# Kernel tuning notes

Measured on AMD Instinct MI355X. Metric: run time of the kernel, lower is better.

## Reference

```python
import jax, jax.numpy as jnp
import numpy as np

N_TREE = 200
DEPTH = 3
N_LEAF = 2 ** (DEPTH + 1) - 1      # 15 internal decision nodes
N_LEAVES = N_LEAF + 1              # 16 leaves
N_NODE = 64
BATCH = 2048
D_FEAT = 512
LR = 0.01


def _leaf_paths(depth):
    """For each of the 2^(depth+1) leaves, the internal-node index and the
    left/right bit at every level (matches the tf.gather index construction:
    bit==0 -> take p, bit==1 -> take 1-p; children of node n are 2n+1, 2n+2)."""
    L = 2 ** (depth + 1)
    nodes = np.zeros((L, depth + 1), np.int32)
    bits = np.zeros((L, depth + 1), np.int32)
    for l in range(L):
        node = 0
        for d in range(depth + 1):
            bit = (l >> (depth - d)) & 1
            nodes[l, d] = node
            bits[l, d] = bit
            node = 2 * node + 1 + bit
    return nodes, bits

_NODES, _BITS = _leaf_paths(DEPTH)


def setup_inputs() -> dict:
    key = jax.random.key(0)
    ks = jax.random.split(key, 9)
    u = lambda k, s: jax.random.uniform(k, s, jnp.float32, -0.05, 0.05)  # keras 'uniform' init
    return {
        "x": jax.random.normal(ks[0], (BATCH, D_FEAT), jnp.float32),
        "y_true": jax.random.normal(ks[1], (BATCH, 1), jnp.float32),
        "w_t": u(ks[2], (N_TREE, D_FEAT, N_NODE)),
        "b_t": u(ks[3], (N_TREE, N_NODE)),
        "w_d": u(ks[4], (N_TREE, N_NODE, N_LEAF)),
        "b_d": u(ks[5], (N_TREE, N_LEAF)),
        "w_l": u(ks[6], (N_TREE, N_LEAVES)),
        "b_l": u(ks[7], (N_TREE,)),
        "f_0": jnp.full((1,), 0.5, jnp.float32),
    }


def reference(x, y_true, w_t, b_t, w_d, b_d, w_l, b_l, f_0):
    B = x.shape[0]
    # Batched per-tree small MLP (the 200-iteration Python loop in the original).
    # Dropout is identity at inference.
    h = jax.nn.relu(jnp.einsum('bd,tdn->tbn', x, w_t) + b_t[:, None, :])        # [T,B,N_NODE]
    p = jax.nn.sigmoid(jnp.einsum('tbn,tnl->tbl', h, w_d) + b_d[:, None, :])    # [T,B,15]
    # Soft binary-tree routing: mu[t,b,leaf] = prod over path of p or (1-p).
    # This reproduces the tiled-index tf.gather construction exactly.
    pn = p[..., _NODES]                                                         # [T,B,16,DEPTH+1]
    q = jnp.where(_BITS == 1, 1.0 - pn, pn)
    mu = jnp.prod(q, axis=-1)                                                   # [T,B,16]
    # Per-tree leaf score with tanh.
    f = jnp.tanh(jnp.einsum('tbl,tl->tb', mu, w_l) + b_l[:, None])              # [T,B]
    # Sequential boosting accumulation: predict_k = f_0 + lr * sum_{i<k} f_i.
    cum = f_0 + LR * jnp.cumsum(f.T, axis=1)                                    # [B,T]
    py_x = jnp.concatenate([jnp.broadcast_to(f_0[None, :], (B, 1)), cum], axis=1)  # [B,T+1]
    return py_x
```

## Files before the change

kernel.cpp:

```cpp
#include <hip/hip_runtime.h>

#define T_TREES 200
#define BATCH   2048
#define D_FEAT  512
#define N_NODE  64
#define LR      0.01f

typedef __attribute__((__ext_vector_type__(8)))  __bf16 bf16x8;
typedef __attribute__((__ext_vector_type__(16))) float  f32x16;

__device__ __forceinline__ unsigned short f32_to_bf16(float f) {
    unsigned u = __float_as_uint(f);
    u += 0x7FFFu + ((u >> 16) & 1u);
    return (unsigned short)(u >> 16);
}

__device__ __forceinline__ void gload_lds16(const void* g, void* l) {
    __builtin_amdgcn_global_load_lds(
        (__attribute__((address_space(1))) void*)(void*)g,
        (__attribute__((address_space(3))) void*)l,
        16, 0, 0);
}

__global__ __launch_bounds__(256) void prep_all(
    const float* __restrict__ x, const float* __restrict__ w_t,
    const float* __restrict__ w_d,
    unsigned short* __restrict__ x_p, unsigned short* __restrict__ w_p,
    unsigned short* __restrict__ w_dt) {
    __shared__ float tile[64 * 65];
    int b = blockIdx.x;
    if (b < 256) {
        int mb = b >> 3, slab = b & 7;
        const float* src = x + (mb * 64) * D_FEAT + slab * 64;
        #pragma unroll
        for (int p = 0; p < 16; ++p) {
            int idx = p * 256 + threadIdx.x;
            int r = idx >> 6, c = idx & 63;
            tile[r * 65 + c] = src[r * D_FEAT + c];
        }
        __syncthreads();
        int mt = mb >> 1, mq = mb & 1;
        unsigned short* dst = x_p + mt * 65536 + slab * 8192 + mq * 512;
        #pragma unroll
        for (int p = 0; p < 2; ++p) {
            int sid = p * 256 + threadIdx.x;
            int kgl = sid >> 6;
            int r   = sid & 63;
            const float* sr = &tile[r * 65 + kgl * 8];
            bf16x8 o;
            #pragma unroll
            for (int j = 0; j < 8; ++j) o[j] = (__bf16)sr[j];
            *(bf16x8*)(dst + kgl * 1024 + r * 8) = o;
        }
    } else if (b < 1856) {
        int bb = b - 256;
        int t = bb >> 3, slab = bb & 7;
        const float* src = w_t + t * (D_FEAT * N_NODE) + slab * 64 * N_NODE;
        #pragma unroll
        for (int p = 0; p < 16; ++p) {
            int idx = p * 256 + threadIdx.x;
            int d = idx >> 6, n = idx & 63;
            tile[d * 65 + n] = src[d * N_NODE + n];
        }
        __syncthreads();
        unsigned short* dst = w_p + (t >> 1) * 65536 + slab * 8192 + (t & 1) * 512;
        #pragma unroll
        for (int p = 0; p < 2; ++p) {
            int sid = p * 256 + threadIdx.x;
            int kgl = sid >> 6;
            int n   = sid & 63;
            bf16x8 o;
            #pragma unroll
            for (int j = 0; j < 8; ++j) o[j] = (__bf16)tile[(kgl * 8 + j) * 65 + n];
            *(bf16x8*)(dst + kgl * 1024 + n * 8) = o;
        }
    } else {
        int i = (b - 1856) * 256 + threadIdx.x;
        int n = i & 63;
        int l = (i >> 6) & 31;
        int t = i >> 11;
        float v = (l < 15) ? w_d[(t * 64 + n) * 15 + l] : 0.f;
        w_dt[i] = f32_to_bf16(v);
    }
}

__global__ __launch_bounds__(256, 4) void gbdt_main(
    const unsigned short* __restrict__ x_p,
    const unsigned short* __restrict__ w_p,
    const unsigned short* __restrict__ w_dt,
    const float* __restrict__ b_t,
    const float* __restrict__ b_d,
    const float* __restrict__ w_l,
    const float* __restrict__ b_l,
    float* __restrict__ f_ws)
{
    __shared__ alignas(16) char smem[34816];
    unsigned short* Hs = (unsigned short*)smem;
    __bf16*         Hb = (__bf16*)smem;
    float*          Pf = (float*)smem;

    const int tid    = threadIdx.x;
    const int lane   = tid & 63;
    const int w      = tid >> 6;
    const int lane31 = lane & 31;
    const int kh     = lane >> 5;
    const int wm     = w >> 1;
    const int wn     = w & 1;

    const int xcd  = blockIdx.x & 7;
    const int slot = blockIdx.x >> 3;
    const int mt   = slot & 15;
    const int pj   = slot >> 4;
    const int pair = xcd * 13 + pj;
    if (pair >= 100) return;
    const int t0 = pair * 2;
    const int m0 = mt * 128;

    const char* ga = (const char*)(x_p + mt * 65536) + tid * 16;
    const char* gb = (const char*)(w_p + pair * 65536) + tid * 16;

    const int aoff = kh * 2048 + (wm * 64 + lane31) * 16;
    const int boff = 8192 + kh * 2048 + (wn * 64 + lane31) * 16;

    f32x16 acc[2][2];
    #pragma unroll
    for (int mb = 0; mb < 2; ++mb)
        #pragma unroll
        for (int nb = 0; nb < 2; ++nb)
            acc[mb][nb] = (f32x16)(0.f);

#define STAGE(cn, base) do {                                              \
        gload_lds16(ga + (cn) * 8192,        (base) + tid * 16);          \
        gload_lds16(ga + (cn) * 8192 + 4096, (base) + tid * 16 + 4096);   \
        gload_lds16(gb + (cn) * 8192,        (base) + 8192 + tid * 16);   \
        gload_lds16(gb + (cn) * 8192 + 4096, (base) + 8192 + tid * 16 + 4096); \
    } while (0)

    STAGE(0, smem);

    for (int c = 0; c < 16; ++c) {
        __syncthreads();
        if (c < 15) STAGE(c + 1, smem + ((c + 1) & 1) * 16384);
        const char* base = smem + (c & 1) * 16384;
        __builtin_amdgcn_s_setprio(1);
        #pragma unroll
        for (int s2 = 0; s2 < 2; ++s2) {
            bf16x8 av0 = *(const bf16x8*)(base + aoff + s2 * 4096);
            bf16x8 av1 = *(const bf16x8*)(base + aoff + s2 * 4096 + 512);
            bf16x8 bv0 = *(const bf16x8*)(base + boff + s2 * 4096);
            bf16x8 bv1 = *(const bf16x8*)(base + boff + s2 * 4096 + 512);
            acc[0][0] = __builtin_amdgcn_mfma_f32_32x32x16_bf16(av0, bv0, acc[0][0], 0, 0, 0);
            acc[0][1] = __builtin_amdgcn_mfma_f32_32x32x16_bf16(av0, bv1, acc[0][1], 0, 0, 0);
            acc[1][0] = __builtin_amdgcn_mfma_f32_32x32x16_bf16(av1, bv0, acc[1][0], 0, 0, 0);
            acc[1][1] = __builtin_amdgcn_mfma_f32_32x32x16_bf16(av1, bv1, acc[1][1], 0, 0, 0);
        }
        __builtin_amdgcn_s_setprio(0);
    }

    __syncthreads();

    #pragma unroll
    for (int nb = 0; nb < 2; ++nb) {
        float btv = b_t[(t0 + wn) * 64 + nb * 32 + lane31];
        #pragma unroll
        for (int mb = 0; mb < 2; ++mb)
            #pragma unroll
            for (int r = 0; r < 16; ++r) {
                int m = wm * 64 + mb * 32 + (r & 3) + 8 * (r >> 2) + 4 * kh;
                float h = fmaxf(acc[mb][nb][r] + btv, 0.f);
                Hb[wn * 8704 + m * 68 + nb * 32 + lane31] = (__bf16)h;
            }
    }
    __syncthreads();

    f32x16 acc2[2] = { (f32x16)(0.f), (f32x16)(0.f) };
    const unsigned short* pW = w_dt + (t0 + wn) * 2048 + lane31 * 64 + kh * 8;
    __builtin_amdgcn_s_setprio(1);
    #pragma unroll
    for (int s = 0; s < 4; ++s) {
        bf16x8 bv = *(const bf16x8*)(pW + s * 16);
        #pragma unroll
        for (int i = 0; i < 2; ++i) {
            const unsigned short* pH =
                Hs + wn * 8704 + (wm * 64 + i * 32 + lane31) * 68 + s * 16 + kh * 8;
            bf16x8 av = *(const bf16x8*)pH;
            acc2[i] = __builtin_amdgcn_mfma_f32_32x32x16_bf16(av, bv, acc2[i], 0, 0, 0);
        }
    }
    __builtin_amdgcn_s_setprio(0);
    __syncthreads();

    if (lane31 < 15) {
        float bdv = b_d[(t0 + wn) * 15 + lane31];
        #pragma unroll
        for (int i = 0; i < 2; ++i)
            #pragma unroll
            for (int r = 0; r < 16; ++r) {
                int m = wm * 64 + i * 32 + (r & 3) + 8 * (r >> 2) + 4 * kh;
                float lg = acc2[i][r] + bdv;
                Pf[(wn * 128 + m) * 17 + lane31] = 1.f / (1.f + __expf(-lg));
            }
    }
    __syncthreads();

    {
        int m = tid & 127;
        int j = tid >> 7;
        int t = t0 + j;
        float pv[15];
        #pragma unroll
        for (int i = 0; i < 15; ++i) pv[i] = Pf[(j * 128 + m) * 17 + i];
        float facc = 0.f;
        #pragma unroll
        for (int leaf = 0; leaf < 16; ++leaf) {
            float mu = 1.f;
            int node = 0;
            #pragma unroll
            for (int d = 0; d < 4; ++d) {
                int bit = (leaf >> (3 - d)) & 1;
                float p = pv[node];
                mu *= bit ? (1.f - p) : p;
                node = 2 * node + 1 + bit;
            }
            facc += mu * w_l[t * 16 + leaf];
        }
        f_ws[(m0 + m) * T_TREES + t] = tanhf(facc + b_l[t]);
    }
#undef STAGE
}

__global__ __launch_bounds__(256) void scan_k(const float* __restrict__ f_ws,
                                              const float* __restrict__ f0p,
                                              float* __restrict__ out) {
    int lane = threadIdx.x & 63, wid = threadIdx.x >> 6;
    int b = blockIdx.x * 4 + wid;
    float f0 = f0p[0];
    float4 v;
    if (lane < 50) v = *(const float4*)(f_ws + b * T_TREES + lane * 4);
    else           v = make_float4(0.f, 0.f, 0.f, 0.f);
    float p0 = v.x;
    float p1 = p0 + v.y;
    float p2 = p1 + v.z;
    float p3 = p2 + v.w;
    float s = p3;
    #pragma unroll
    for (int off = 1; off < 64; off <<= 1) {
        float y = __shfl_up(s, off, 64);
        if (lane >= off) s += y;
    }
    float excl = s - p3;
    if (lane < 50) {
        float* o = out + b * (T_TREES + 1) + 1 + lane * 4;
        o[0] = f0 + LR * (excl + p0);
        o[1] = f0 + LR * (excl + p1);
        o[2] = f0 + LR * (excl + p2);
        o[3] = f0 + LR * (excl + p3);
    }
    if (lane == 0) out[b * (T_TREES + 1)] = f0;
}

extern "C" void kernel_launch(void* const* d_in, const int* in_sizes, int n_in,
                              void* d_out, int out_size, void* d_ws, size_t ws_size,
                              hipStream_t stream) {
    const float* x   = (const float*)d_in[0];
    const float* w_t = (const float*)d_in[2];
    const float* b_t = (const float*)d_in[3];
    const float* w_d = (const float*)d_in[4];
    const float* b_d = (const float*)d_in[5];
    const float* w_l = (const float*)d_in[6];
    const float* b_l = (const float*)d_in[7];
    const float* f_0 = (const float*)d_in[8];
    float* out = (float*)d_out;

    char* ws = (char*)d_ws;
    unsigned short* x_p  = (unsigned short*)(ws);
    unsigned short* w_p  = (unsigned short*)(ws + 2097152);
    unsigned short* w_dt = (unsigned short*)(ws + 15204352);
    float*          f_ws = (float*)(ws + 16023552);

    prep_all<<<3456, 256, 0, stream>>>(x, w_t, w_d, x_p, w_p, w_dt);
    gbdt_main<<<1664, 256, 0, stream>>>(x_p, w_p, w_dt, b_t, b_d, w_l, b_l, f_ws);
    scan_k<<<512, 256, 0, stream>>>(f_ws, f_0, out);
}
```

Measured before the change: 133.0 us.

## Double block M-tile to 256 rows and add triple-buffered K pipeline

Each block now has 512 threads and covers 256 batch rows per tree pair instead of 128. Each tree's weight tile is therefore staged once for twice as many rows, halving weight traffic per output. The K loop switches from a double buffer with __syncthreads to a three-stage LDS ring of 64-wide K chunks. It uses explicit vmcnt waits and a single barrier, keeping two chunks in flight. The cost is 144 KB of LDS per block, which allows only one block per CU, and half as many blocks in the grid, so there is less latency hiding from concurrent blocks.

```diff
diff --git a/kernel.cpp b/kernel.cpp
--- a/kernel.cpp
+++ b/kernel.cpp
@@ -84,7 +84,7 @@
     }
 }
 
-__global__ __launch_bounds__(256, 4) void gbdt_main(
+__global__ __launch_bounds__(512, 2) void gbdt_main(
     const unsigned short* __restrict__ x_p,
     const unsigned short* __restrict__ w_p,
     const unsigned short* __restrict__ w_dt,
@@ -94,7 +94,7 @@
     const float* __restrict__ b_l,
     float* __restrict__ f_ws)
 {
-    __shared__ alignas(16) char smem[34816];
+    __shared__ alignas(16) char smem[147456];
     unsigned short* Hs = (unsigned short*)smem;
     __bf16*         Hb = (__bf16*)smem;
     float*          Pf = (float*)smem;
@@ -109,18 +109,19 @@
 
     const int xcd  = blockIdx.x & 7;
     const int slot = blockIdx.x >> 3;
-    const int mt   = slot & 15;
-    const int pj   = slot >> 4;
+    const int mt8  = slot & 7;
+    const int pj   = slot >> 3;
     const int pair = xcd * 13 + pj;
     if (pair >= 100) return;
     const int t0 = pair * 2;
-    const int m0 = mt * 128;
-
-    const char* ga = (const char*)(x_p + mt * 65536) + tid * 16;
-    const char* gb = (const char*)(w_p + pair * 65536) + tid * 16;
-
-    const int aoff = kh * 2048 + (wm * 64 + lane31) * 16;
-    const int boff = 8192 + kh * 2048 + (wn * 64 + lane31) * 16;
+    const int m0 = mt8 * 256;
+
+    const char* ga0 = (const char*)(x_p + (2 * mt8 + 0) * 65536) + tid * 16;
+    const char* ga1 = (const char*)(x_p + (2 * mt8 + 1) * 65536) + tid * 16;
+    const char* gb  = (const char*)(w_p + pair * 65536) + tid * 16;
+
+    const int aoff = (wm >> 1) * 16384 + kh * 2048 + ((wm & 1) * 64 + lane31) * 16;
+    const int boff = 32768 + kh * 2048 + (wn * 64 + lane31) * 16;
 
     f32x16 acc[2][2];
     #pragma unroll
@@ -129,32 +130,42 @@
         for (int nb = 0; nb < 2; ++nb)
             acc[mb][nb] = (f32x16)(0.f);
 
-#define STAGE(cn, base) do {                                              \
-        gload_lds16(ga + (cn) * 8192,        (base) + tid * 16);          \
-        gload_lds16(ga + (cn) * 8192 + 4096, (base) + tid * 16 + 4096);   \
-        gload_lds16(gb + (cn) * 8192,        (base) + 8192 + tid * 16);   \
-        gload_lds16(gb + (cn) * 8192 + 4096, (base) + 8192 + tid * 16 + 4096); \
+#define STAGE(kt, base) do {                                               \
+        gload_lds16(ga0 + (kt) * 16384,        (base) + tid * 16);         \
+        gload_lds16(ga0 + (kt) * 16384 + 8192, (base) + 8192  + tid * 16); \
+        gload_lds16(ga1 + (kt) * 16384,        (base) + 16384 + tid * 16); \
+        gload_lds16(ga1 + (kt) * 16384 + 8192, (base) + 24576 + tid * 16); \
+        gload_lds16(gb  + (kt) * 16384,        (base) + 32768 + tid * 16); \
+        gload_lds16(gb  + (kt) * 16384 + 8192, (base) + 40960 + tid * 16); \
     } while (0)
 
-    STAGE(0, smem);
-
-    for (int c = 0; c < 16; ++c) {
-        __syncthreads();
-        if (c < 15) STAGE(c + 1, smem + ((c + 1) & 1) * 16384);
-        const char* base = smem + (c & 1) * 16384;
+    char* b0 = smem;
+    char* b1 = smem + 49152;
+    char* b2 = smem + 98304;
+
+    STAGE(0, b0);
+    STAGE(1, b1);
+
+    #pragma unroll
+    for (int kt = 0; kt < 8; ++kt) {
+        if (kt < 7) asm volatile("s_waitcnt vmcnt(6)" ::: "memory");
+        else        asm volatile("s_waitcnt vmcnt(0)" ::: "memory");
+        __builtin_amdgcn_s_barrier();
+        if (kt < 6) STAGE(kt + 2, b2);
         __builtin_amdgcn_s_setprio(1);
         #pragma unroll
-        for (int s2 = 0; s2 < 2; ++s2) {
-            bf16x8 av0 = *(const bf16x8*)(base + aoff + s2 * 4096);
-            bf16x8 av1 = *(const bf16x8*)(base + aoff + s2 * 4096 + 512);
-            bf16x8 bv0 = *(const bf16x8*)(base + boff + s2 * 4096);
-            bf16x8 bv1 = *(const bf16x8*)(base + boff + s2 * 4096 + 512);
+        for (int ks = 0; ks < 4; ++ks) {
+            bf16x8 av0 = *(const bf16x8*)(b0 + aoff + ks * 4096);
+            bf16x8 av1 = *(const bf16x8*)(b0 + aoff + ks * 4096 + 512);
+            bf16x8 bv0 = *(const bf16x8*)(b0 + boff + ks * 4096);
+            bf16x8 bv1 = *(const bf16x8*)(b0 + boff + ks * 4096 + 512);
             acc[0][0] = __builtin_amdgcn_mfma_f32_32x32x16_bf16(av0, bv0, acc[0][0], 0, 0, 0);
             acc[0][1] = __builtin_amdgcn_mfma_f32_32x32x16_bf16(av0, bv1, acc[0][1], 0, 0, 0);
             acc[1][0] = __builtin_amdgcn_mfma_f32_32x32x16_bf16(av1, bv0, acc[1][0], 0, 0, 0);
             acc[1][1] = __builtin_amdgcn_mfma_f32_32x32x16_bf16(av1, bv1, acc[1][1], 0, 0, 0);
         }
         __builtin_amdgcn_s_setprio(0);
+        char* t = b0; b0 = b1; b1 = b2; b2 = t;
     }
 
     __syncthreads();
@@ -167,8 +178,8 @@
             #pragma unroll
             for (int r = 0; r < 16; ++r) {
                 int m = wm * 64 + mb * 32 + (r & 3) + 8 * (r >> 2) + 4 * kh;
-                float h = fmaxf(acc[mb][nb][r] + btv, 0.f);
-                Hb[wn * 8704 + m * 68 + nb * 32 + lane31] = (__bf16)h;
+                float hv = fmaxf(acc[mb][nb][r] + btv, 0.f);
+                Hb[(wn * 256 + m) * 68 + nb * 32 + lane31] = (__bf16)hv;
             }
     }
     __syncthreads();
@@ -182,7 +193,7 @@
         #pragma unroll
         for (int i = 0; i < 2; ++i) {
             const unsigned short* pH =
-                Hs + wn * 8704 + (wm * 64 + i * 32 + lane31) * 68 + s * 16 + kh * 8;
+                Hs + (wn * 256 + wm * 64 + i * 32 + lane31) * 68 + s * 16 + kh * 8;
             bf16x8 av = *(const bf16x8*)pH;
             acc2[i] = __builtin_amdgcn_mfma_f32_32x32x16_bf16(av, bv, acc2[i], 0, 0, 0);
         }
@@ -198,18 +209,18 @@
             for (int r = 0; r < 16; ++r) {
                 int m = wm * 64 + i * 32 + (r & 3) + 8 * (r >> 2) + 4 * kh;
                 float lg = acc2[i][r] + bdv;
-                Pf[(wn * 128 + m) * 17 + lane31] = 1.f / (1.f + __expf(-lg));
+                Pf[(wn * 256 + m) * 17 + lane31] = 1.f / (1.f + __expf(-lg));
             }
     }
     __syncthreads();
 
     {
-        int m = tid & 127;
-        int j = tid >> 7;
+        int m = tid & 255;
+        int j = tid >> 8;
         int t = t0 + j;
         float pv[15];
         #pragma unroll
-        for (int i = 0; i < 15; ++i) pv[i] = Pf[(j * 128 + m) * 17 + i];
+        for (int i = 0; i < 15; ++i) pv[i] = Pf[(j * 256 + m) * 17 + i];
         float facc = 0.f;
         #pragma unroll
         for (int leaf = 0; leaf < 16; ++leaf) {
@@ -279,6 +290,6 @@
     float*          f_ws = (float*)(ws + 16023552);
 
     prep_all<<<3456, 256, 0, stream>>>(x, w_t, w_d, x_p, w_p, w_dt);
-    gbdt_main<<<1664, 256, 0, stream>>>(x_p, w_p, w_dt, b_t, b_d, w_l, b_l, f_ws);
+    gbdt_main<<<832, 512, 0, stream>>>(x_p, w_p, w_dt, b_t, b_d, w_l, b_l, f_ws);
     scan_k<<<512, 256, 0, stream>>>(f_ws, f_0, out);
 }
```

Result: slower. 146.5 us (+10.1%).
